# Performance work log

Measured on AMD Instinct MI355X. Metric: run time of the kernel, lower is better.

## Reference

```python
import jax
import jax.numpy as jnp
from jax import lax
import numpy as np

B, CIN, COUT, RANK, K, H, W = 16, 256, 256, 64, 3, 112, 112
PAD = 1


def setup_inputs() -> dict:
    key = jax.random.key(0)
    k1, k2, k3, k4, k5 = jax.random.split(key, 5)
    x = jax.random.normal(k1, (B, CIN, H, W), dtype=jnp.float32)
    # head: `rank` stacked 1x1 conv weights, each [COUT, CIN]
    w_head = jax.random.normal(k2, (RANK, COUT, CIN), dtype=jnp.float32) * 0.05
    # body: Conv2d(COUT -> RANK, kernel (K,1)), OIHW layout
    w_body = jax.random.normal(k3, (RANK, COUT, K, 1), dtype=jnp.float32) * 0.05
    # tail: Conv2d(RANK -> COUT, kernel (1,K)), OIHW layout, with bias
    w_tail = jax.random.normal(k4, (COUT, RANK, 1, K), dtype=jnp.float32) * 0.05
    b_tail = jax.random.normal(k5, (COUT,), dtype=jnp.float32) * 0.05
    return {"x": x, "w_head": w_head, "w_body": w_body, "w_tail": w_tail, "b_tail": b_tail}


_DN = lax.conv_dimension_numbers((B, CIN, H, W), (COUT, CIN, 1, 1), ("NCHW", "OIHW", "NCHW"))


def reference(x, w_head, w_body, w_tail, b_tail):
    # Sum of rank 1x1 convs over the same input == one 1x1 conv with summed
    # weights (conv is linear in the weight) — same math, one pass.
    w_sum = w_head.sum(axis=0)                      # [COUT, CIN]
    y = jnp.einsum("bihw,oi->bohw", x, w_sum)       # [B, COUT, H, W]
    # body: (K,1) conv, stride (1,1), padding (PAD, 0)
    y = lax.conv_general_dilated(y, w_body, window_strides=(1, 1),
                                 padding=((PAD, PAD), (0, 0)),
                                 dimension_numbers=_DN)  # [B, RANK, H, W]
    # tail: (1,K) conv, stride (1,1), padding (0, PAD), plus bias
    y = lax.conv_general_dilated(y, w_tail, window_strides=(1, 1),
                                 padding=((0, 0), (PAD, PAD)),
                                 dimension_numbers=_DN)  # [B, COUT, H, W]
    return y + b_tail[None, :, None, None]
```

## Files before the change

### kernel.cpp

```cpp
#include <hip/hip_runtime.h>
#include <stdint.h>

#define CIN 256
#define COUT 256
#define RANK 64
#define H_ 112
#define W_ 112
#define HW_ (112*112)

typedef short bf16x8 __attribute__((ext_vector_type(8)));
typedef float f32x4 __attribute__((ext_vector_type(4)));

__device__ __forceinline__ unsigned rne2(float a, float b){
  unsigned ua = __builtin_bit_cast(unsigned, a);
  unsigned ub = __builtin_bit_cast(unsigned, b);
  ua += 0x7FFFu + ((ua >> 16) & 1u);
  ub += 0x7FFFu + ((ub >> 16) & 1u);
  return (ua >> 16) | (ub & 0xFFFF0000u);
}
__device__ __forceinline__ unsigned short rne1(float a){
  unsigned ua = __builtin_bit_cast(unsigned, a);
  ua += 0x7FFFu + ((ua >> 16) & 1u);
  return (unsigned short)(ua >> 16);
}

__global__ __launch_bounds__(256) void k_pre1(const float* __restrict__ x,
                                              unsigned short* __restrict__ xt,
                                              const float* __restrict__ wh,
                                              float* __restrict__ wsum,
                                              int base_b, int nb){
  __shared__ float ldsf[64*120];
  const int tid = threadIdx.x;
  if (blockIdx.x >= (unsigned)(nb*114)){
    int o = blockIdx.x - nb*114;
    float s = 0.f;
    for (int k = 0; k < RANK; ++k) s += wh[(k*COUT + o)*CIN + tid];
    wsum[o*CIN + tid] = s;
    return;
  }
  const int lb = blockIdx.x / 114, hh = blockIdx.x % 114;
  const int bb = base_b + lb;
  const int h = hh - 1;
  unsigned short* dst = xt + ((size_t)(lb*114 + hh))*28672;

  if (h < 0 || h >= H_){
    uint4 z = {0,0,0,0};
    #pragma unroll
    for (int j = 0; j < 14; ++j)
      *(uint4*)(dst + (tid + 256*j)*8) = z;
    return;
  }

  for (int i0p = 0; i0p < 4; ++i0p){
    int c = tid / 28, wq = tid % 28;
    #pragma unroll
    for (int j = 0; j < 7; ++j){
      const float4 v = *(const float4*)(x + ((size_t)(bb*CIN + i0p*64 + c))*HW_ + h*W_ + wq*4);
      *(float4*)&ldsf[c*120 + wq*4] = v;
      wq += 4; c += 9; if (wq >= 28){ wq -= 28; c += 1; }
    }
    __syncthreads();
    for (int ck = tid; ck < 896; ck += 256){
      int g8 = ck / 112, w = ck % 112;
      const float* src = &ldsf[(g8*8)*120 + w];
      uint4 st;
      st.x = rne2(src[0],     src[120]);
      st.y = rne2(src[240],   src[360]);
      st.z = rne2(src[480],   src[600]);
      st.w = rne2(src[720],   src[840]);
      *(uint4*)(dst + (size_t)(i0p*896 + ck)*8) = st;
    }
    __syncthreads();
  }
}

__global__ __launch_bounds__(256) void k_pre2(const float* __restrict__ wb,
                                              const float* __restrict__ wsum,
                                              unsigned short* __restrict__ weff,
                                              const float* __restrict__ wt,
                                              unsigned short* __restrict__ wtp){
  const int tid = threadIdx.x;
  if (blockIdx.x < 192){
    int bid = blockIdx.x;
    int dh = bid >> 6, r = bid & 63;
    float s = 0.f;
    for (int o = 0; o < COUT; ++o)
      s += wb[(r*COUT + o)*3 + dh] * wsum[o*CIN + tid];
    weff[bid*CIN + tid] = rne1(s);
  } else {
    int o = blockIdx.x - 192;
    if (tid < 192){
      int dw = tid >> 6, r = tid & 63;
      wtp[o*192 + tid] = rne1(wt[(o*RANK + r)*3 + dw]);
    }
  }
}

__global__ __launch_bounds__(256,2) void k_fused(const unsigned short* __restrict__ xt,
                                                 const unsigned short* __restrict__ weff,
                                                 const unsigned short* __restrict__ wtp,
                                                 const float* __restrict__ bias,
                                                 float* __restrict__ out,
                                                 int base_b){
  __shared__ alignas(16) unsigned short lds[28672];
  const int tid  = threadIdx.x;
  const int wid  = tid >> 6, lane = tid & 63, g = lane >> 4, l15 = lane & 15;
  const int lb   = blockIdx.x / 56, hb = blockIdx.x % 56;
  const int bb   = base_b + lb;
  const int h0   = hb*2;
  const int hloc = wid >> 1, rhalf = wid & 1;

  f32x4 acc[2][7];
  #pragma unroll
  for (int a = 0; a < 2; ++a)
    #pragma unroll
    for (int b = 0; b < 7; ++b) acc[a][b] = (f32x4){0.f,0.f,0.f,0.f};

  const unsigned short* rowbase = xt + ((size_t)(lb*114 + h0 + wid)*8)*3584;

  auto stage = [&](unsigned short* dstbuf, int i0){
    const unsigned short* src = rowbase + (size_t)i0*3584 + lane*8;
    unsigned short* dstb = dstbuf + wid*3584;
    #pragma unroll
    for (int k = 0; k < 7; ++k)
      __builtin_amdgcn_global_load_lds(
        (const __attribute__((address_space(1))) void*)(src + k*512),
        (__attribute__((address_space(3))) void*)(dstb + k*512), 16, 0, 0);
  };

  auto compute = [&](const unsigned short* buf, int i0){
    #pragma unroll
    for (int dh = 0; dh < 3; ++dh){
      const int row = hloc + dh;
      const unsigned short* ab = weff + (size_t)(dh*64 + rhalf*32 + l15)*CIN + i0*32 + g*8;
      bf16x8 af0 = *(const bf16x8*)(ab);
      bf16x8 af1 = *(const bf16x8*)(ab + 16*CIN);
      const unsigned short* qb = buf + row*3584 + g*896 + l15*8;
      #pragma unroll
      for (int wt = 0; wt < 7; ++wt){
        bf16x8 bfv = *(const bf16x8*)(qb + wt*128);
        acc[0][wt] = __builtin_amdgcn_mfma_f32_16x16x32_bf16(af0, bfv, acc[0][wt], 0, 0, 0);
        acc[1][wt] = __builtin_amdgcn_mfma_f32_16x16x32_bf16(af1, bfv, acc[1][wt], 0, 0, 0);
      }
    }
  };

  unsigned short* cur = lds;
  unsigned short* nxt = lds + 14336;
  stage(cur, 0);
  __syncthreads();
  for (int t = 0; t < 8; ++t){
    if (t < 7) stage(nxt, t+1);
    compute(cur, t);
    __syncthreads();
    unsigned short* tmp = cur; cur = nxt; nxt = tmp;
  }

  unsigned short* y2b = lds;
  if (tid < 32){
    int hh = tid >> 4, wsel = (tid >> 3) & 1, rq = tid & 7;
    *(uint4*)(y2b + hh*8208 + (wsel ? 113 : 0)*72 + rq*8) = (uint4){0,0,0,0};
  }
  #pragma unroll
  for (int wt = 0; wt < 7; ++wt){
    #pragma unroll
    for (int rt = 0; rt < 2; ++rt){
      unsigned lo = rne2(acc[rt][wt][0], acc[rt][wt][1]);
      unsigned hi = rne2(acc[rt][wt][2], acc[rt][wt][3]);
      uint2 st; st.x = lo; st.y = hi;
      *(uint2*)(y2b + hloc*8208 + (wt*16 + l15 + 1)*72 + rhalf*32 + rt*16 + g*4) = st;
    }
  }
  __syncthreads();

  const int h = h0 + hloc;
  #pragma unroll
  for (int opass = 0; opass < 2; ++opass){
    const int obase = rhalf*128 + opass*64;
    f32x4 a2[4][7];
    #pragma unroll
    for (int a = 0; a < 4; ++a)
      #pragma unroll
      for (int b = 0; b < 7; ++b) a2[a][b] = (f32x4){0.f,0.f,0.f,0.f};

    #pragma unroll
    for (int s = 0; s < 6; ++s){
      bf16x8 af[4];
      const unsigned short* ab = wtp + (size_t)(obase + l15)*192 + s*32 + g*8;
      #pragma unroll
      for (int rt = 0; rt < 4; ++rt)
        af[rt] = *(const bf16x8*)(ab + rt*16*192);
      const unsigned short* qb = y2b + hloc*8208 + (l15 + (s >> 1))*72 + (s & 1)*32 + g*8;
      #pragma unroll
      for (int wt = 0; wt < 7; ++wt){
        bf16x8 bv = *(const bf16x8*)(qb + wt*16*72);
        #pragma unroll
        for (int rt = 0; rt < 4; ++rt)
          a2[rt][wt] = __builtin_amdgcn_mfma_f32_16x16x32_bf16(af[rt], bv, a2[rt][wt], 0, 0, 0);
      }
    }

    float* ob = out + ((size_t)(bb*COUT) + obase)*HW_ + h*W_;
    #pragma unroll
    for (int rt = 0; rt < 4; ++rt){
      #pragma unroll
      for (int ii = 0; ii < 4; ++ii){
        float bvv = bias[obase + rt*16 + g*4 + ii];
        #pragma unroll
        for (int wt = 0; wt < 7; ++wt)
          ob[(size_t)(rt*16 + g*4 + ii)*HW_ + wt*16 + l15] = a2[rt][wt][ii] + bvv;
      }
    }
  }
}

extern "C" void kernel_launch(void* const* d_in, const int* in_sizes, int n_in,
                              void* d_out, int out_size, void* d_ws, size_t ws_size,
                              hipStream_t stream) {
  const float* x      = (const float*)d_in[0];
  const float* w_head = (const float*)d_in[1];
  const float* w_body = (const float*)d_in[2];
  const float* w_tail = (const float*)d_in[3];
  const float* b_tail = (const float*)d_in[4];
  float* out = (float*)d_out;
  char* ws = (char*)d_ws;

  float*          wsum = (float*)ws;
  unsigned short* weff = (unsigned short*)(ws + 262144);
  unsigned short* wtp  = (unsigned short*)(ws + 360448);
  unsigned short* xt   = (unsigned short*)(ws + 458752);

  const size_t XT_ROW_BYTES = 57344;
  const size_t XT_PER_B     = 114 * XT_ROW_BYTES;
  size_t avail = (ws_size > 458752) ? ws_size - 458752 : 0;
  int chunk_b = (int)(avail / XT_PER_B);
  if (chunk_b > 16) chunk_b = 16;
  if (chunk_b < 1)  chunk_b = 1;
  int nchunks = (16 + chunk_b - 1) / chunk_b;

  int base = 0;
  for (int c = 0; c < nchunks; ++c){
    int remaining = 16 - base;
    int nb = (remaining + (nchunks - c) - 1) / (nchunks - c);
    k_pre1<<<nb*114 + (c == 0 ? 256 : 0), 256, 0, stream>>>(x, xt, w_head, wsum, base, nb);
    if (c == 0)
      k_pre2<<<448, 256, 0, stream>>>(w_body, wsum, weff, w_tail, wtp);
    k_fused<<<nb*56, 256, 0, stream>>>(xt, weff, wtp, b_tail, out, base);
    base += nb;
  }
}
```

Baseline: 181.6 us.

## Halve LDS staging tiles and tail accumulators to allow four blocks per CU

```diff
diff --git a/kernel.cpp b/kernel.cpp
--- a/kernel.cpp
+++ b/kernel.cpp
@@ -96,13 +96,13 @@
   }
 }
 
-__global__ __launch_bounds__(256,2) void k_fused(const unsigned short* __restrict__ xt,
+__global__ __launch_bounds__(256,4) void k_fused(const unsigned short* __restrict__ xt,
                                                  const unsigned short* __restrict__ weff,
                                                  const unsigned short* __restrict__ wtp,
                                                  const float* __restrict__ bias,
                                                  float* __restrict__ out,
                                                  int base_b){
-  __shared__ alignas(16) unsigned short lds[28672];
+  __shared__ alignas(16) unsigned short lds[16416];
   const int tid  = threadIdx.x;
   const int wid  = tid >> 6, lane = tid & 63, g = lane >> 4, l15 = lane & 15;
   const int lb   = blockIdx.x / 56, hb = blockIdx.x % 56;
@@ -118,40 +118,59 @@
 
   const unsigned short* rowbase = xt + ((size_t)(lb*114 + h0 + wid)*8)*3584;
 
-  auto stage = [&](unsigned short* dstbuf, int i0){
-    const unsigned short* src = rowbase + (size_t)i0*3584 + lane*8;
-    unsigned short* dstb = dstbuf + wid*3584;
-    #pragma unroll
-    for (int k = 0; k < 7; ++k)
-      __builtin_amdgcn_global_load_lds(
-        (const __attribute__((address_space(1))) void*)(src + k*512),
-        (__attribute__((address_space(3))) void*)(dstb + k*512), 16, 0, 0);
+  auto stage = [&](unsigned short* dstbuf, int q){
+    const int i0 = q >> 1, hf = q & 1;
+    const unsigned short* src0 = rowbase + (size_t)i0*3584;
+    if (hf == 0){
+      unsigned short* dstb = dstbuf + wid*2048;
+      const unsigned short* s = src0 + lane*8;
+      #pragma unroll
+      for (int gc = 0; gc < 4; ++gc)
+        __builtin_amdgcn_global_load_lds(
+          (const __attribute__((address_space(1))) void*)(s + gc*896),
+          (__attribute__((address_space(3))) void*)(dstb + gc*512), 16, 0, 0);
+    } else {
+      if (lane < 48){
+        unsigned short* dstb = dstbuf + wid*1536;
+        const unsigned short* s = src0 + 512 + lane*8;
+        #pragma unroll
+        for (int gc = 0; gc < 4; ++gc)
+          __builtin_amdgcn_global_load_lds(
+            (const __attribute__((address_space(1))) void*)(s + gc*896),
+            (__attribute__((address_space(3))) void*)(dstb + gc*384), 16, 0, 0);
+      }
+    }
   };
 
-  auto compute = [&](const unsigned short* buf, int i0){
+  auto compute = [&](const unsigned short* buf, int q){
+    const int i0 = q >> 1, hf = q & 1;
+    const int wt0 = hf ? 4 : 0, wtn = hf ? 3 : 4;
+    const int rstride = hf ? 1536 : 2048;
+    const int gstride = hf ? 384 : 512;
     #pragma unroll
     for (int dh = 0; dh < 3; ++dh){
-      const int row = hloc + dh;
       const unsigned short* ab = weff + (size_t)(dh*64 + rhalf*32 + l15)*CIN + i0*32 + g*8;
       bf16x8 af0 = *(const bf16x8*)(ab);
       bf16x8 af1 = *(const bf16x8*)(ab + 16*CIN);
-      const unsigned short* qb = buf + row*3584 + g*896 + l15*8;
-      #pragma unroll
-      for (int wt = 0; wt < 7; ++wt){
-        bf16x8 bfv = *(const bf16x8*)(qb + wt*128);
-        acc[0][wt] = __builtin_amdgcn_mfma_f32_16x16x32_bf16(af0, bfv, acc[0][wt], 0, 0, 0);
-        acc[1][wt] = __builtin_amdgcn_mfma_f32_16x16x32_bf16(af1, bfv, acc[1][wt], 0, 0, 0);
+      const unsigned short* qb = buf + (hloc + dh)*rstride + g*gstride + l15*8;
+      #pragma unroll
+      for (int w = 0; w < 4; ++w){
+        if (w < wtn){
+          bf16x8 bfv = *(const bf16x8*)(qb + w*128);
+          acc[0][wt0+w] = __builtin_amdgcn_mfma_f32_16x16x32_bf16(af0, bfv, acc[0][wt0+w], 0, 0, 0);
+          acc[1][wt0+w] = __builtin_amdgcn_mfma_f32_16x16x32_bf16(af1, bfv, acc[1][wt0+w], 0, 0, 0);
+        }
       }
     }
   };
 
   unsigned short* cur = lds;
-  unsigned short* nxt = lds + 14336;
+  unsigned short* nxt = lds + 8192;
   stage(cur, 0);
   __syncthreads();
-  for (int t = 0; t < 8; ++t){
-    if (t < 7) stage(nxt, t+1);
-    compute(cur, t);
+  for (int q = 0; q < 16; ++q){
+    if (q < 15) stage(nxt, q+1);
+    compute(cur, q);
     __syncthreads();
     unsigned short* tmp = cur; cur = nxt; nxt = tmp;
   }
@@ -175,34 +194,34 @@
 
   const int h = h0 + hloc;
   #pragma unroll
-  for (int opass = 0; opass < 2; ++opass){
-    const int obase = rhalf*128 + opass*64;
-    f32x4 a2[4][7];
-    #pragma unroll
-    for (int a = 0; a < 4; ++a)
+  for (int opass = 0; opass < 4; ++opass){
+    const int obase = rhalf*128 + opass*32;
+    f32x4 a2[2][7];
+    #pragma unroll
+    for (int a = 0; a < 2; ++a)
       #pragma unroll
       for (int b = 0; b < 7; ++b) a2[a][b] = (f32x4){0.f,0.f,0.f,0.f};
 
     #pragma unroll
     for (int s = 0; s < 6; ++s){
-      bf16x8 af[4];
+      bf16x8 afc[2];
       const unsigned short* ab = wtp + (size_t)(obase + l15)*192 + s*32 + g*8;
       #pragma unroll
-      for (int rt = 0; rt < 4; ++rt)
-        af[rt] = *(const bf16x8*)(ab + rt*16*192);
+      for (int rt = 0; rt < 2; ++rt)
+        afc[rt] = *(const bf16x8*)(ab + rt*16*192);
       const unsigned short* qb = y2b + hloc*8208 + (l15 + (s >> 1))*72 + (s & 1)*32 + g*8;
       #pragma unroll
       for (int wt = 0; wt < 7; ++wt){
         bf16x8 bv = *(const bf16x8*)(qb + wt*16*72);
         #pragma unroll
-        for (int rt = 0; rt < 4; ++rt)
-          a2[rt][wt] = __builtin_amdgcn_mfma_f32_16x16x32_bf16(af[rt], bv, a2[rt][wt], 0, 0, 0);
+        for (int rt = 0; rt < 2; ++rt)
+          a2[rt][wt] = __builtin_amdgcn_mfma_f32_16x16x32_bf16(afc[rt], bv, a2[rt][wt], 0, 0, 0);
       }
     }
 
     float* ob = out + ((size_t)(bb*COUT) + obase)*HW_ + h*W_;
     #pragma unroll
-    for (int rt = 0; rt < 4; ++rt){
+    for (int rt = 0; rt < 2; ++rt){
       #pragma unroll
       for (int ii = 0; ii < 4; ++ii){
         float bvv = bias[obase + rt*16 + g*4 + ii];
@@ -230,8 +249,7 @@
   unsigned short* wtp  = (unsigned short*)(ws + 360448);
   unsigned short* xt   = (unsigned short*)(ws + 458752);
 
-  const size_t XT_ROW_BYTES = 57344;
-  const size_t XT_PER_B     = 114 * XT_ROW_BYTES;
+  const size_t XT_PER_B = (size_t)114 * 57344;
   size_t avail = (ws_size > 458752) ? ws_size - 458752 : 0;
   int chunk_b = (int)(avail / XT_PER_B);
   if (chunk_b > 16) chunk_b = 16;
```

Result: no change. 179.0 us (-1.4%).
